# Kernel tuning notes

Hardware: AMD Instinct MI355X
Metric: run time of the kernel (lower is better)

## Reference

```python
import jax, jax.numpy as jnp
import numpy as np

MARGIN = 0.2
EPS = 1e-8
N, D_EMB, N_CLASSES = 8192, 256, 512


def setup_inputs() -> dict:
    key = jax.random.key(0)
    k1, k2 = jax.random.split(key)
    embeddings = jax.random.normal(k1, (N, D_EMB), dtype=jnp.float32)
    labels = jax.random.randint(k2, (N,), 0, N_CLASSES, dtype=jnp.int64)
    return {"embeddings": embeddings, "labels": labels}


def reference(embeddings, labels):
    # OnlineTripleLoss.forward with sampling_strategy='fixed_semi_hard', cosine metric.
    n = embeddings.shape[0]
    norms = jnp.linalg.norm(embeddings, axis=1, keepdims=True)
    xn = embeddings / jnp.maximum(norms, EPS)
    dist = 1.0 - xn @ xn.T                       # [N, N] cosine distance

    same = labels[:, None] == labels[None, :]    # same-label mask
    neg_mask = ~same
    has_neg = jnp.any(neg_mask, axis=1)          # anchor has at least one negative

    # fixed_semi_hard argmax(ap+margin-an) == argmin(an); fallback is also argmin(an)
    BIG = jnp.float32(1e9)
    dmin_neg = jnp.min(jnp.where(neg_mask, dist, BIG), axis=1)  # [N]

    # all anchor-positive combinations: same label, a < p (itertools.combinations order)
    upper = jnp.triu(jnp.ones((n, n), dtype=bool), 1)
    pair_mask = same & upper & has_neg[:, None]

    losses = jnp.maximum(dist - dmin_neg[:, None] + MARGIN, 0.0)
    count = jnp.sum(pair_mask)
    loss_sum = jnp.sum(jnp.where(pair_mask, losses, 0.0))
    loss = jnp.where(count > 0, loss_sum / jnp.maximum(count, 1).astype(jnp.float32), 0.0)
    return loss, count
```

## Files before the change

### kernel.cpp

```cpp
#include <hip/hip_runtime.h>
#include <hip/hip_bf16.h>

#define NROWS 8192
#define DEMB 256
#define MARGIN 0.2f
#define NCLS 512
#define NCAP 96
#define TPC 8
#define NSTEP 16

typedef __attribute__((ext_vector_type(4))) float f32x4;
typedef __attribute__((ext_vector_type(8))) short bf16x8;

static __device__ __forceinline__ unsigned short f2b(float f) {
    unsigned u = __builtin_bit_cast(unsigned, f);
    u += 0x7fffu + ((u >> 16) & 1u);
    return (unsigned short)(u >> 16);
}
static __device__ __forceinline__ float b2f(unsigned short b) {
    unsigned u = ((unsigned)b) << 16;
    return __builtin_bit_cast(float, u);
}
static __device__ __forceinline__ unsigned encf(float f) {
    unsigned u = __builtin_bit_cast(unsigned, f);
    return (u & 0x80000000u) ? ~u : (u | 0x80000000u);
}
static __device__ __forceinline__ float decf(unsigned e) {
    unsigned u = (e & 0x80000000u) ? (e ^ 0x80000000u) : ~e;
    return __builtin_bit_cast(float, u);
}
static __device__ __forceinline__ void gload16(const void* g, void* l) {
    __builtin_amdgcn_global_load_lds(
        (const __attribute__((address_space(1))) unsigned int*)g,
        (__attribute__((address_space(3))) unsigned int*)l, 16, 0, 0);
}

__global__ __launch_bounds__(256) void k_norm(const float* __restrict__ x,
                                              unsigned short* __restrict__ xnb,
                                              unsigned* __restrict__ amax) {
    int gid = blockIdx.x * blockDim.x + threadIdx.x;
    if (gid < NROWS) amax[gid] = 0u;
    int row  = gid >> 6;
    int lane = threadIdx.x & 63;
    const float4* p = reinterpret_cast<const float4*>(x + (size_t)row * DEMB) + lane;
    float4 v = *p;
    float s = v.x * v.x + v.y * v.y + v.z * v.z + v.w * v.w;
#pragma unroll
    for (int m = 1; m < 64; m <<= 1) s += __shfl_xor(s, m);
    float inv = 1.0f / fmaxf(sqrtf(s), 1e-8f);
    ushort4 o;
    o.x = f2b(v.x * inv); o.y = f2b(v.y * inv);
    o.z = f2b(v.z * inv); o.w = f2b(v.w * inv);
    *(reinterpret_cast<ushort4*>(xnb + (size_t)row * DEMB) + lane) = o;
}

__global__ __launch_bounds__(512, 2) void k_maxneg(const unsigned short* __restrict__ xnb,
                                                   const int* __restrict__ labels,
                                                   unsigned* __restrict__ amax) {
    extern __shared__ char lds[];
    unsigned short* Bl = (unsigned short*)lds;

    int tid  = threadIdx.x;
    int wid  = tid >> 6, lane = tid & 63;
    int wr   = wid >> 1, wc = wid & 1;
    int arow = lane & 15, kgrp = lane >> 4;

    int i0 = blockIdx.x * 128;
    int j0 = blockIdx.y * (TPC * 128);

    bf16x8 a[2][8];
    const unsigned short* ap0 = xnb + (size_t)(i0 + wr * 32 + arow) * DEMB + kgrp * 8;
#pragma unroll
    for (int m = 0; m < 2; ++m)
#pragma unroll
        for (int kk = 0; kk < 8; ++kk)
            a[m][kk] = *(const bf16x8*)(ap0 + m * 16 * DEMB + kk * 32);

    int rlab[2][4];
#pragma unroll
    for (int m = 0; m < 2; ++m)
#pragma unroll
        for (int r = 0; r < 4; ++r)
            rlab[m][r] = labels[i0 + wr * 32 + m * 16 + kgrp * 4 + r];

    float rmax[2][4] = {{-1e30f, -1e30f, -1e30f, -1e30f},
                        {-1e30f, -1e30f, -1e30f, -1e30f}};
    f32x4 acc[2][4] = {};

    auto stage = [&](int buf, int t, int h) {
#pragma unroll
        for (int is = 0; is < 4; ++is) {
            int idx  = is * 512 + tid;
            int row  = idx >> 4;
            int colb = (idx & 15) << 4;
            int scol = (colb ^ ((row & 15) << 4)) >> 1;
            const unsigned short* src =
                xnb + (size_t)(j0 + t * 128 + row) * DEMB + h * 128 + scol;
            unsigned short* dst = Bl + buf * 16384 + is * 4096 + wid * 512;
            gload16(src, dst);
        }
    };

    int clab[4], nlab[4];
    stage(0, 0, 0);
#pragma unroll
    for (int n = 0; n < 4; ++n) clab[n] = labels[j0 + wc * 64 + n * 16 + arow];

    int sw = arow << 4;
    for (int s = 0; s < NSTEP; ++s) {
        __syncthreads();
        if (s + 1 < NSTEP) stage((s + 1) & 1, (s + 1) >> 1, (s + 1) & 1);
        int tile = s >> 1, h = s & 1;
        if (h == 0 && tile + 1 < TPC) {
#pragma unroll
            for (int n = 0; n < 4; ++n)
                nlab[n] = labels[j0 + (tile + 1) * 128 + wc * 64 + n * 16 + arow];
        }
        const char* Bt = (const char*)(Bl + (s & 1) * 16384);
        bf16x8 b[4][4];
#pragma unroll
        for (int n = 0; n < 4; ++n) {
            int rb = (wc * 64 + n * 16 + arow) * 256;
#pragma unroll
            for (int ksl = 0; ksl < 4; ++ksl)
                b[n][ksl] = *(const bf16x8*)(Bt + rb + ((ksl * 64 + kgrp * 16) ^ sw));
        }
#pragma unroll
        for (int m = 0; m < 2; ++m)
#pragma unroll
            for (int n = 0; n < 4; ++n)
#pragma unroll
                for (int ksl = 0; ksl < 4; ++ksl)
                    acc[m][n] = __builtin_amdgcn_mfma_f32_16x16x32_bf16(
                        a[m][h * 4 + ksl], b[n][ksl], acc[m][n], 0, 0, 0);
        if (h == 1) {
#pragma unroll
            for (int m = 0; m < 2; ++m)
#pragma unroll
                for (int r = 0; r < 4; ++r) {
                    float v = rmax[m][r];
                    int rl = rlab[m][r];
#pragma unroll
                    for (int n = 0; n < 4; ++n)
                        if (clab[n] != rl) v = fmaxf(v, acc[m][n][r]);
                    rmax[m][r] = v;
                }
#pragma unroll
            for (int m = 0; m < 2; ++m)
#pragma unroll
                for (int n = 0; n < 4; ++n) acc[m][n] = (f32x4){0.f, 0.f, 0.f, 0.f};
#pragma unroll
            for (int n = 0; n < 4; ++n) clab[n] = nlab[n];
        }
    }

    float* smax = (float*)Bl;
#pragma unroll
    for (int m = 0; m < 2; ++m)
#pragma unroll
        for (int r = 0; r < 4; ++r) {
            float v = rmax[m][r];
#pragma unroll
            for (int msk = 1; msk < 16; msk <<= 1) v = fmaxf(v, __shfl_xor(v, msk));
            if (arow == 0) smax[wc * 128 + wr * 32 + m * 16 + kgrp * 4 + r] = v;
        }
    __syncthreads();
    if (tid < 128) {
        float v = fmaxf(smax[tid], smax[128 + tid]);
        if (v > -1e29f) atomicMax(amax + i0 + tid, encf(v));
    }
}

__global__ __launch_bounds__(256) void k_cpairs(const unsigned short* __restrict__ xnb,
                                                const int* __restrict__ labels,
                                                const unsigned* __restrict__ amax,
                                                float* __restrict__ closs,
                                                int* __restrict__ ccnt) {
    extern __shared__ char lds2[];
    unsigned short* srows = (unsigned short*)lds2;
    __shared__ int clist[NCAP];
    __shared__ float sdm[NCAP];
    __shared__ unsigned char shn[NCAP];
    __shared__ unsigned short pl[NCAP * (NCAP - 1) / 2];
    __shared__ int wcnt[4], woff[4], snc;
    __shared__ float slloss[16];
    __shared__ int slcnt[16];

    int c   = blockIdx.x;
    int tid = threadIdx.x, wid = tid >> 6, lane = tid & 63;

    int base = wid * 2048;
    int cnt = 0;
    for (int s = 0; s < 8; ++s) {
        int b0 = base + s * 256;
#pragma unroll
        for (int e = 0; e < 4; ++e)
            cnt += __popcll(__ballot(labels[b0 + e * 64 + lane] == c));
    }
    if (lane == 0) wcnt[wid] = cnt;
    __syncthreads();
    if (tid == 0) {
        int o = 0;
        for (int w = 0; w < 4; ++w) { woff[w] = o; o += wcnt[w]; }
        snc = (o > NCAP) ? NCAP : o;
    }
    __syncthreads();
    int nc = snc;

    int off = woff[wid];
    for (int s = 0; s < 8; ++s) {
        int b0 = base + s * 256;
#pragma unroll
        for (int e = 0; e < 4; ++e) {
            int idx = b0 + e * 64 + lane;
            bool hit = (labels[idx] == c);
            unsigned long long m = __ballot(hit);
            int rank = __popcll(m & ((1ull << lane) - 1ull));
            if (hit && off + rank < NCAP) clist[off + rank] = idx;
            off += __popcll(m);
        }
    }
    __syncthreads();

    int nch = nc * 32;
    for (int ch = tid; ch < nch; ch += 256) {
        int r = ch >> 5, cc = ch & 31;
        *(bf16x8*)(srows + r * 256 + cc * 8) =
            *(const bf16x8*)(xnb + (size_t)clist[r] * DEMB + cc * 8);
    }
    if (tid < nc) {
        unsigned e = amax[clist[tid]];
        shn[tid] = (e != 0u);
        sdm[tid] = 1.0f - decf(e);
    }
    int npairs = nc * (nc - 1) / 2;
    for (int p = tid; p < npairs; p += 256) {
        int i = 0, rem = p;
        while (rem >= nc - 1 - i) { rem -= nc - 1 - i; ++i; }
        pl[p] = (unsigned short)((i << 8) | (i + 1 + rem));
    }
    __syncthreads();

    int slot = tid >> 4, gl = tid & 15;
    float gloss = 0.f;
    int gcnt = 0;
    for (int p = slot; p < npairs; p += 16) {
        int pr = pl[p], i = pr >> 8, j = pr & 255;
        bf16x8 a0 = *(const bf16x8*)(srows + i * 256 + gl * 16);
        bf16x8 a1 = *(const bf16x8*)(srows + i * 256 + gl * 16 + 8);
        bf16x8 b0 = *(const bf16x8*)(srows + j * 256 + gl * 16);
        bf16x8 b1 = *(const bf16x8*)(srows + j * 256 + gl * 16 + 8);
        float dot = 0.f;
#pragma unroll
        for (int e = 0; e < 8; ++e) {
            dot += b2f((unsigned short)a0[e]) * b2f((unsigned short)b0[e]);
            dot += b2f((unsigned short)a1[e]) * b2f((unsigned short)b1[e]);
        }
#pragma unroll
        for (int msk = 1; msk < 16; msk <<= 1) dot += __shfl_xor(dot, msk);
        if (gl == 0 && shn[i]) {
            gloss += fmaxf(1.0f - dot - sdm[i] + MARGIN, 0.0f);
            gcnt += 1;
        }
    }
    if (gl == 0) { slloss[slot] = gloss; slcnt[slot] = gcnt; }
    __syncthreads();
    if (tid == 0) {
        float s = 0.f; int k = 0;
        for (int q = 0; q < 16; ++q) { s += slloss[q]; k += slcnt[q]; }
        closs[c] = s; ccnt[c] = k;
    }
}

__global__ __launch_bounds__(256) void k_final(const float* __restrict__ closs,
                                               const int* __restrict__ ccnt,
                                               float* __restrict__ out) {
    __shared__ float sl[256];
    __shared__ int   sc[256];
    int tid = threadIdx.x;
    float s = closs[tid] + closs[tid + 256];
    int   k = ccnt[tid] + ccnt[tid + 256];
    sl[tid] = s; sc[tid] = k;
    __syncthreads();
    for (int st = 128; st > 0; st >>= 1) {
        if (tid < st) {
            sl[tid] += sl[tid + st];
            sc[tid] += sc[tid + st];
        }
        __syncthreads();
    }
    if (tid == 0) {
        out[0] = (sc[0] > 0) ? sl[0] / (float)sc[0] : 0.0f;
        out[1] = (float)sc[0];
    }
}

extern "C" void kernel_launch(void* const* d_in, const int* in_sizes, int n_in,
                              void* d_out, int out_size, void* d_ws, size_t ws_size,
                              hipStream_t stream) {
    const float* emb  = (const float*)d_in[0];
    const int* labels = (const int*)d_in[1];
    float* out = (float*)d_out;

    char* ws = (char*)d_ws;
    unsigned short* xnb = (unsigned short*)ws;
    unsigned* amax = (unsigned*)(ws + (size_t)4 * 1024 * 1024);
    float* closs   = (float*)   (ws + (size_t)4 * 1024 * 1024 + 32768);
    int*   ccnt    = (int*)     (ws + (size_t)4 * 1024 * 1024 + 40960);

    k_norm<<<NROWS / 4, 256, 0, stream>>>(emb, xnb, amax);
    dim3 g2(NROWS / 128, NCLS / 64);
    k_maxneg<<<g2, 512, 65536, stream>>>(xnb, labels, amax);
    k_cpairs<<<NCLS, 256, 49152, stream>>>(xnb, labels, amax, closs, ccnt);
    k_final<<<1, 256, 0, stream>>>(closs, ccnt, out);
}
```

Baseline: 81.77 us.

## Bucket rows by label with atomics instead of per-class label scans

Adds a k_bucket kernel that uses atomicAdd to assign each row to a per-class member list, so the per-class pair kernel no longer scans all 8192 labels twice per block. The pair kernel reads its member list directly, pads LDS rows to reduce bank conflicts, and computes pair indices inline instead of building a pair table. Because atomic ordering is nondeterministic, the anchor is chosen as the lower global index of the pair. This adds an extra launch, and classes with more than 64 members (previously 96) would be truncated.

```diff
diff --git a/kernel.cpp b/kernel.cpp
--- a/kernel.cpp
+++ b/kernel.cpp
@@ -5,9 +5,10 @@
 #define DEMB 256
 #define MARGIN 0.2f
 #define NCLS 512
-#define NCAP 96
 #define TPC 8
 #define NSTEP 16
+#define MCAP 64
+#define SROW 264
 
 typedef __attribute__((ext_vector_type(4))) float f32x4;
 typedef __attribute__((ext_vector_type(8))) short bf16x8;
@@ -37,9 +38,11 @@
 
 __global__ __launch_bounds__(256) void k_norm(const float* __restrict__ x,
                                               unsigned short* __restrict__ xnb,
-                                              unsigned* __restrict__ amax) {
+                                              unsigned* __restrict__ amax,
+                                              int* __restrict__ bcnt) {
     int gid = blockIdx.x * blockDim.x + threadIdx.x;
     if (gid < NROWS) amax[gid] = 0u;
+    if (gid < NCLS) bcnt[gid] = 0;
     int row  = gid >> 6;
     int lane = threadIdx.x & 63;
     const float4* p = reinterpret_cast<const float4*>(x + (size_t)row * DEMB) + lane;
@@ -52,6 +55,17 @@
     o.x = f2b(v.x * inv); o.y = f2b(v.y * inv);
     o.z = f2b(v.z * inv); o.w = f2b(v.w * inv);
     *(reinterpret_cast<ushort4*>(xnb + (size_t)row * DEMB) + lane) = o;
+}
+
+__global__ __launch_bounds__(256) void k_bucket(const int* __restrict__ labels,
+                                                int* __restrict__ bcnt,
+                                                int* __restrict__ mem) {
+    int i = blockIdx.x * 256 + threadIdx.x;
+    if (i < NROWS) {
+        int l = labels[i];
+        int slot = atomicAdd(&bcnt[l], 1);
+        if (slot < MCAP) mem[l * MCAP + slot] = i;
+    }
 }
 
 __global__ __launch_bounds__(512, 2) void k_maxneg(const unsigned short* __restrict__ xnb,
@@ -171,85 +185,52 @@
     }
 }
 
-__global__ __launch_bounds__(256) void k_cpairs(const unsigned short* __restrict__ xnb,
-                                                const int* __restrict__ labels,
-                                                const unsigned* __restrict__ amax,
-                                                float* __restrict__ closs,
-                                                int* __restrict__ ccnt) {
-    extern __shared__ char lds2[];
-    unsigned short* srows = (unsigned short*)lds2;
-    __shared__ int clist[NCAP];
-    __shared__ float sdm[NCAP];
-    __shared__ unsigned char shn[NCAP];
-    __shared__ unsigned short pl[NCAP * (NCAP - 1) / 2];
-    __shared__ int wcnt[4], woff[4], snc;
+__global__ __launch_bounds__(256) void k_cpairs2(const unsigned short* __restrict__ xnb,
+                                                 const unsigned* __restrict__ amax,
+                                                 const int* __restrict__ bcnt,
+                                                 const int* __restrict__ mem,
+                                                 float* __restrict__ closs,
+                                                 int* __restrict__ ccnt) {
+    __shared__ unsigned short srows[MCAP * SROW];
+    __shared__ int mlist[MCAP];
+    __shared__ float sdm[MCAP];
+    __shared__ unsigned char shn[MCAP];
     __shared__ float slloss[16];
     __shared__ int slcnt[16];
 
     int c   = blockIdx.x;
-    int tid = threadIdx.x, wid = tid >> 6, lane = tid & 63;
-
-    int base = wid * 2048;
-    int cnt = 0;
-    for (int s = 0; s < 8; ++s) {
-        int b0 = base + s * 256;
-#pragma unroll
-        for (int e = 0; e < 4; ++e)
-            cnt += __popcll(__ballot(labels[b0 + e * 64 + lane] == c));
-    }
-    if (lane == 0) wcnt[wid] = cnt;
-    __syncthreads();
-    if (tid == 0) {
-        int o = 0;
-        for (int w = 0; w < 4; ++w) { woff[w] = o; o += wcnt[w]; }
-        snc = (o > NCAP) ? NCAP : o;
-    }
-    __syncthreads();
-    int nc = snc;
-
-    int off = woff[wid];
-    for (int s = 0; s < 8; ++s) {
-        int b0 = base + s * 256;
-#pragma unroll
-        for (int e = 0; e < 4; ++e) {
-            int idx = b0 + e * 64 + lane;
-            bool hit = (labels[idx] == c);
-            unsigned long long m = __ballot(hit);
-            int rank = __popcll(m & ((1ull << lane) - 1ull));
-            if (hit && off + rank < NCAP) clist[off + rank] = idx;
-            off += __popcll(m);
-        }
-    }
-    __syncthreads();
-
+    int tid = threadIdx.x;
+    int nc  = bcnt[c];
+    if (nc > MCAP) nc = MCAP;
+
+    if (tid < nc) {
+        int gi = mem[c * MCAP + tid];
+        mlist[tid] = gi;
+        unsigned e = amax[gi];
+        shn[tid] = (e != 0u);
+        sdm[tid] = 1.0f - decf(e);
+    }
+    __syncthreads();
     int nch = nc * 32;
     for (int ch = tid; ch < nch; ch += 256) {
         int r = ch >> 5, cc = ch & 31;
-        *(bf16x8*)(srows + r * 256 + cc * 8) =
-            *(const bf16x8*)(xnb + (size_t)clist[r] * DEMB + cc * 8);
-    }
-    if (tid < nc) {
-        unsigned e = amax[clist[tid]];
-        shn[tid] = (e != 0u);
-        sdm[tid] = 1.0f - decf(e);
-    }
+        *(bf16x8*)(srows + r * SROW + cc * 8) =
+            *(const bf16x8*)(xnb + (size_t)mlist[r] * DEMB + cc * 8);
+    }
+    __syncthreads();
+
+    int slot = tid >> 4, gl = tid & 15;
     int npairs = nc * (nc - 1) / 2;
-    for (int p = tid; p < npairs; p += 256) {
-        int i = 0, rem = p;
-        while (rem >= nc - 1 - i) { rem -= nc - 1 - i; ++i; }
-        pl[p] = (unsigned short)((i << 8) | (i + 1 + rem));
-    }
-    __syncthreads();
-
-    int slot = tid >> 4, gl = tid & 15;
     float gloss = 0.f;
     int gcnt = 0;
     for (int p = slot; p < npairs; p += 16) {
-        int pr = pl[p], i = pr >> 8, j = pr & 255;
-        bf16x8 a0 = *(const bf16x8*)(srows + i * 256 + gl * 16);
-        bf16x8 a1 = *(const bf16x8*)(srows + i * 256 + gl * 16 + 8);
-        bf16x8 b0 = *(const bf16x8*)(srows + j * 256 + gl * 16);
-        bf16x8 b1 = *(const bf16x8*)(srows + j * 256 + gl * 16 + 8);
+        int i = 0, rem = p;
+        while (rem >= nc - 1 - i) { rem -= nc - 1 - i; ++i; }
+        int j = i + 1 + rem;
+        bf16x8 a0 = *(const bf16x8*)(srows + i * SROW + gl * 16);
+        bf16x8 a1 = *(const bf16x8*)(srows + i * SROW + gl * 16 + 8);
+        bf16x8 b0 = *(const bf16x8*)(srows + j * SROW + gl * 16);
+        bf16x8 b1 = *(const bf16x8*)(srows + j * SROW + gl * 16 + 8);
         float dot = 0.f;
 #pragma unroll
         for (int e = 0; e < 8; ++e) {
@@ -258,9 +239,12 @@
         }
 #pragma unroll
         for (int msk = 1; msk < 16; msk <<= 1) dot += __shfl_xor(dot, msk);
-        if (gl == 0 && shn[i]) {
-            gloss += fmaxf(1.0f - dot - sdm[i] + MARGIN, 0.0f);
-            gcnt += 1;
+        if (gl == 0) {
+            int ai = (mlist[i] < mlist[j]) ? i : j;
+            if (shn[ai]) {
+                gloss += fmaxf(1.0f - dot - sdm[ai] + MARGIN, 0.0f);
+                gcnt += 1;
+            }
         }
     }
     if (gl == 0) { slloss[slot] = gloss; slcnt[slot] = gcnt; }
@@ -305,12 +289,15 @@
     char* ws = (char*)d_ws;
     unsigned short* xnb = (unsigned short*)ws;
     unsigned* amax = (unsigned*)(ws + (size_t)4 * 1024 * 1024);
-    float* closs   = (float*)   (ws + (size_t)4 * 1024 * 1024 + 32768);
-    int*   ccnt    = (int*)     (ws + (size_t)4 * 1024 * 1024 + 40960);
-
-    k_norm<<<NROWS / 4, 256, 0, stream>>>(emb, xnb, amax);
+    int* bcnt = (int*)(ws + (size_t)4 * 1024 * 1024 + 32768);
+    int* mem  = (int*)(ws + (size_t)4 * 1024 * 1024 + 34816);
+    float* closs = (float*)(ws + (size_t)4 * 1024 * 1024 + 34816 + 131072);
+    int*   ccnt  = (int*)  (ws + (size_t)4 * 1024 * 1024 + 34816 + 131072 + 2048);
+
+    k_norm<<<NROWS / 4, 256, 0, stream>>>(emb, xnb, amax, bcnt);
+    k_bucket<<<NROWS / 256, 256, 0, stream>>>(labels, bcnt, mem);
     dim3 g2(NROWS / 128, NCLS / 64);
     k_maxneg<<<g2, 512, 65536, stream>>>(xnb, labels, amax);
-    k_cpairs<<<NCLS, 256, 49152, stream>>>(xnb, labels, amax, closs, ccnt);
+    k_cpairs2<<<NCLS, 256, 0, stream>>>(xnb, amax, bcnt, mem, closs, ccnt);
     k_final<<<1, 256, 0, stream>>>(closs, ccnt, out);
 }
```

Result: faster. 80.13 us (-2.0%).
